# Kernel tuning notes

Measured on AMD Instinct MI355X. Metric: run time of the kernel, lower is better.

Reference implementation:

```python
import jax, jax.numpy as jnp
import numpy as np

H = 16           # num_heads
D = 1024         # num_units
QD = KD = VD = 64
LN_EPS = 1e-5


def _xavier(key, shape):
    fan_in, fan_out = shape[-2], shape[-1]
    std = np.sqrt(2.0 / (fan_in + fan_out))
    return jax.random.normal(key, shape, dtype=jnp.float32) * std


def setup_inputs() -> dict:
    key = jax.random.key(0)
    ks = jax.random.split(key, 10)
    B, Sq, Sk = 8, 1024, 1024
    return {
        "query": jax.random.normal(ks[0], (B, Sq, D), dtype=jnp.float32),
        "keys": jax.random.normal(ks[1], (B, Sk, D), dtype=jnp.float32),
        "values": jax.random.normal(ks[2], (B, Sk, D), dtype=jnp.float32),
        "Wq": _xavier(ks[3], (H, D, QD)),
        "Wk": _xavier(ks[4], (H, D, KD)),
        "Wv": _xavier(ks[5], (H, D, VD)),
        "Wp": _xavier(ks[6], (H * VD, D)),   # proj, stored input-major: y = x @ Wp + bp
        "bp": jnp.zeros((D,), dtype=jnp.float32),
        "gamma": jnp.ones((D,), dtype=jnp.float32),
        "beta": jnp.zeros((D,), dtype=jnp.float32),
    }


def reference(query, keys, values, Wq, Wk, Wv, Wp, bp, gamma, beta):
    B, Sq, _ = query.shape
    Sk = keys.shape[1]
    # RepeatLinear per head: [B,S,D] x [H,D,e] -> [H,B,S,e]
    Q = jnp.einsum("bsd,hde->hbse", query, Wq)
    K = jnp.einsum("bsd,hde->hbse", keys, Wk)
    V = jnp.einsum("bsd,hde->hbse", values, Wv)
    # NOTE: original scales by sqrt(num_units), not sqrt(key_dim)
    temper = jnp.asarray(np.sqrt(D), dtype=Q.dtype)
    scores = jnp.einsum("hbqe,hbke->hbqk", Q, K) / temper  # [H,B,Sq,Sk]
    attn = jax.nn.softmax(scores, axis=-1)
    # dropout is identity in eval mode
    out = jnp.einsum("hbqk,hbke->hbqe", attn, V)           # [H,B,Sq,VD]
    # torch.cat(torch.split(out, B, 0), -1): head-major feature concat
    out = out.transpose(1, 2, 0, 3).reshape(B, Sq, H * VD)
    out = out @ Wp + bp                                     # proj
    # residual + LayerNorm
    y = out + query
    mu = jnp.mean(y, axis=-1, keepdims=True)
    var = jnp.var(y, axis=-1, keepdims=True)
    y = (y - mu) / jnp.sqrt(var + LN_EPS) * gamma + beta
    return y, attn.reshape(H * B, Sq, Sk)
```

## Files before the change

### kernel.cpp

```cpp
#include <hip/hip_runtime.h>
#include <hip/hip_bf16.h>

#define H_ 16
#define B_ 8
#define S_ 1024
#define D_ 1024
#define E_ 64
#define HB_ 128
#define LN_EPS 1e-5f
#define LOG2E 1.4426950408889634f

typedef unsigned short u16;
typedef __bf16 bf16x8 __attribute__((ext_vector_type(8)));
typedef u16 u16x8 __attribute__((ext_vector_type(8)));
typedef u16 u16x4 __attribute__((ext_vector_type(4)));
typedef float f32x4 __attribute__((ext_vector_type(4)));
typedef unsigned u32x2 __attribute__((ext_vector_type(2)));

#define MFMA16(a, b, c) __builtin_amdgcn_mfma_f32_16x16x32_bf16( \
    __builtin_bit_cast(bf16x8, (a)), __builtin_bit_cast(bf16x8, (b)), (c), 0, 0, 0)

#define GLL16(gp, lp) __builtin_amdgcn_global_load_lds( \
    (const __attribute__((address_space(1))) void*)(gp), \
    (__attribute__((address_space(3))) void*)(lp), 16, 0, 0)

__device__ __forceinline__ unsigned cvt_pk_bf16(float lo, float hi) {
  unsigned r;
  asm("v_cvt_pk_bf16_f32 %0, %1, %2" : "=v"(r) : "v"(lo), "v"(hi));
  return r;
}
__device__ __forceinline__ u16x4 pk4(f32x4 v) {
  union { unsigned u[2]; u16x4 s; } r;
  r.u[0] = cvt_pk_bf16(v[0], v[1]);
  r.u[1] = cvt_pk_bf16(v[2], v[3]);
  return r.s;
}
__device__ __forceinline__ float exp2_hw(float x) {
  float r;
  asm("v_exp_f32 %0, %1" : "=v"(r) : "v"(x));
  return r;
}
__device__ __forceinline__ float bfhi(unsigned u) {
  return __builtin_bit_cast(float, u & 0xFFFF0000u);
}
__device__ __forceinline__ float bflo(unsigned u) {
  return __builtin_bit_cast(float, u << 16);
}

__global__ __launch_bounds__(256) void k_prep(
    const float* __restrict__ Wq, const float* __restrict__ Wk,
    const float* __restrict__ Wv, const float* __restrict__ Wp,
    u16* __restrict__ Wt,
    const float* __restrict__ Xq, const float* __restrict__ Xk,
    const float* __restrict__ Xv, u16* __restrict__ Xdst) {
  const int bid = blockIdx.x;
  if (bid >= 1024) {
    const int b2 = bid - 1024;
    const int t = b2 >> 12;
    const float* X = t == 0 ? Xq : t == 1 ? Xk : Xv;
    u16* Y = Xdst + (size_t)t * (8 << 20);
    int i = ((b2 & 4095) * 256 + threadIdx.x) * 8;
    f32x4 a = *(const f32x4*)(X + i);
    f32x4 b = *(const f32x4*)(X + i + 4);
    union { unsigned u[4]; u16x8 s; } v;
    v.u[0] = cvt_pk_bf16(a[0], a[1]);
    v.u[1] = cvt_pk_bf16(a[2], a[3]);
    v.u[2] = cvt_pk_bf16(b[0], b[1]);
    v.u[3] = cvt_pk_bf16(b[2], b[3]);
    *(u16x8*)(Y + i) = v.s;
    return;
  }
  __shared__ float tile[64][65];
  const int which = bid >> 8, r = bid & 255;
  const float* src;
  int R, C, rt, ct;
  float scale = 1.0f;
  size_t soff, doff;
  if (which < 3) {
    src = which == 0 ? Wq : which == 1 ? Wk : Wv;
    if (which == 0) scale = LOG2E / 32.0f;
    int slice = r & 15, rtile = r >> 4;
    R = 1024; C = 64; rt = rtile * 64; ct = 0;
    soff = (size_t)slice * 65536;
    doff = (size_t)which * (1 << 20) + (size_t)slice * 65536;
  } else {
    src = Wp;
    R = 1024; C = 1024; rt = (r & 15) * 64; ct = (r >> 4) * 64;
    soff = 0; doff = (size_t)3 * (1 << 20);
  }
  const float* I = src + soff;
  u16* O = Wt + doff;
  const int t = threadIdx.x;
  const int c4 = (t & 15) * 4;
  #pragma unroll
  for (int i = 0; i < 4; i++) {
    int rr = i * 16 + (t >> 4);
    f32x4 v = *(const f32x4*)&I[(size_t)(rt + rr) * C + ct + c4];
    tile[rr][c4 + 0] = v[0]; tile[rr][c4 + 1] = v[1];
    tile[rr][c4 + 2] = v[2]; tile[rr][c4 + 3] = v[3];
  }
  __syncthreads();
  #pragma unroll
  for (int i = 0; i < 4; i++) {
    int oc = i * 16 + (t >> 4);
    f32x4 tv;
    #pragma unroll
    for (int rr = 0; rr < 4; rr++) tv[rr] = tile[c4 + rr][oc] * scale;
    *(u16x4*)&O[(size_t)(ct + oc) * R + rt + c4] = pk4(tv);
  }
}

#define STAGE_TILES() do { \
    GLL16(Ag + kt,             AsB0); \
    GLL16(Ag + 64 * 1024 + kt, AsB0 + 2048); \
    GLL16(Bg + kt,             BsB0); \
    GLL16(Bg + 64 * 1024 + kt, BsB0 + 2048); \
  } while (0)

#define READ_FRAGS() do { \
    _Pragma("unroll") \
    for (int mi = 0; mi < 4; mi++) \
      af[mi] = *(const u16x8*)&As[(wr * 64 + mi * 16 + lr) * 32 + lg * 8]; \
    _Pragma("unroll") \
    for (int ni = 0; ni < 4; ni++) \
      bf[ni] = *(const u16x8*)&Bs[(wc * 64 + ni * 16 + lr) * 32 + lg * 8]; \
  } while (0)

template<int MODE>
__global__ __launch_bounds__(256) void k_gemm(
    const u16* __restrict__ X0, const u16* __restrict__ Ball,
    u16* __restrict__ O0, u16* __restrict__ O1, u16* __restrict__ O2,
    float* __restrict__ Pf, const float* __restrict__ bp,
    const float* __restrict__ query) {
  const int bid = blockIdx.x + (blockIdx.y << 6);
  const int bx  = ((bid & 7) << 3) + ((bid >> 3) & 7);
  const int by  = bid >> 6;
  const int l  = threadIdx.x & 63;
  const int w  = threadIdx.x >> 6;
  const int lr = l & 15, lg = l >> 4;
  const int wr = w >> 1, wc = w & 1;
  const int m0 = bx * 128, n0 = by * 128;

  const u16* A = (MODE == 0) ? X0 + (size_t)(by >> 3) * (8 << 20) : X0;

  __shared__ __align__(16) u16 As[128 * 32];
  __shared__ __align__(16) u16 Bs[128 * 32];

  const int srow = w * 16 + (l >> 2);
  const int scol = (l & 3) * 8;
  const u16* Ag = A    + (size_t)(m0 + srow) * 1024 + scol;
  const u16* Bg = Ball + (size_t)(n0 + srow) * 1024 + scol;
  u16* AsB0 = As + w * 512;
  u16* BsB0 = Bs + w * 512;

  f32x4 acc[4][4] = {};
  u16x8 af[4], bf[4];

  if (MODE == 2 || by < 16) {
    for (int kt = 0; kt < 1024; kt += 32) {
      STAGE_TILES();
      __syncthreads();
      READ_FRAGS();
      #pragma unroll
      for (int mi = 0; mi < 4; mi++)
        #pragma unroll
        for (int ni = 0; ni < 4; ni++)
          acc[mi][ni] = MFMA16(bf[ni], af[mi], acc[mi][ni]);
      __syncthreads();
    }
  } else {
    for (int kt = 0; kt < 1024; kt += 32) {
      STAGE_TILES();
      __syncthreads();
      READ_FRAGS();
      #pragma unroll
      for (int mi = 0; mi < 4; mi++)
        #pragma unroll
        for (int ni = 0; ni < 4; ni++)
          acc[mi][ni] = MFMA16(af[mi], bf[ni], acc[mi][ni]);
      __syncthreads();
    }
  }

  if (MODE == 0 && by < 16) {
    u16* Out = (by >= 8) ? O1 : O0;
    const int h = (by & 7) * 2 + wc;
    #pragma unroll
    for (int mi = 0; mi < 4; mi++) {
      int s = m0 + wr * 64 + mi * 16 + lr;
      int bb = s >> 10, ss = s & 1023;
      #pragma unroll
      for (int ni = 0; ni < 4; ni++)
        *(u16x4*)&Out[((size_t)(h * 8 + bb) * 1024 + ss) * 64 + ni * 16 + lg * 4] =
            pk4(acc[mi][ni]);
    }
  } else if (MODE == 0) {
    const int byv = by - 16;
    const int h = byv * 2 + wc;
    #pragma unroll
    for (int mi = 0; mi < 4; mi++) {
      int s = m0 + wr * 64 + mi * 16 + lg * 4;
      int bb = s >> 10, ss = s & 1023;
      #pragma unroll
      for (int ni = 0; ni < 4; ni++)
        *(u16x4*)&O2[((size_t)(h * 8 + bb) * 64 + ni * 16 + lr) * 1024 + ss] =
            pk4(acc[mi][ni]);
    }
  } else {
    #pragma unroll
    for (int mi = 0; mi < 4; mi++) {
      int m = m0 + wr * 64 + mi * 16 + lr;
      #pragma unroll
      for (int ni = 0; ni < 4; ni++) {
        int n = n0 + wc * 64 + ni * 16 + lg * 4;
        f32x4 b4 = *(const f32x4*)(bp + n);
        f32x4 q4 = *(const f32x4*)(query + (size_t)m * 1024 + n);
        f32x4 o = acc[mi][ni] + b4 + q4;
        *(f32x4*)(Pf + (size_t)m * 1024 + n) = o;
      }
    }
  }
}

__global__ __launch_bounds__(256, 4) void k_attn(const u16* __restrict__ Qb,
    const u16* __restrict__ Kb, const u16* __restrict__ Vtb,
    float* __restrict__ attn_out, u16* __restrict__ AO) {
  const int bid = blockIdx.x;
  const int xcd = bid & 7, within = bid >> 3;
  const int qt = within & 63;
  const int hb = xcd * 16 + (within >> 6);
  const int w  = threadIdx.x >> 6;
  const int l  = threadIdx.x & 63;
  const int lr = l & 15, lg = l >> 4;
  const int q0 = qt * 16;

  __shared__ __align__(16) u16 pbuf[16 * 1024];
  __shared__ float wmaxs[4][16];
  __shared__ float wsums[4][16];

  const u16* Qp = Qb + ((size_t)hb * 1024 + q0 + lr) * 64 + lg * 8;
  const u16* Kp = Kb + ((size_t)hb * 1024 + w * 256 + lr) * 64 + lg * 8;
  u16x8 q_lo = *(const u16x8*)Qp;
  u16x8 q_hi = *(const u16x8*)(Qp + 32);

  f32x4 sacc[16] = {};
  __builtin_amdgcn_s_setprio(1);
  #pragma unroll
  for (int j = 0; j < 16; j++) {
    u16x8 k0 = *(const u16x8*)(Kp + (size_t)j * 16 * 64);
    u16x8 k1 = *(const u16x8*)(Kp + (size_t)j * 16 * 64 + 32);
    sacc[j] = MFMA16(k0, q_lo, sacc[j]);
    sacc[j] = MFMA16(k1, q_hi, sacc[j]);
  }
  __builtin_amdgcn_s_setprio(0);

  float mx = sacc[0][0];
  #pragma unroll
  for (int j = 0; j < 16; j++)
    #pragma unroll
    for (int r = 0; r < 4; r++) mx = fmaxf(mx, sacc[j][r]);
  mx = fmaxf(mx, __shfl_xor(mx, 16));
  mx = fmaxf(mx, __shfl_xor(mx, 32));

  float sum = 0.f;
  #pragma unroll
  for (int j = 0; j < 16; j++)
    #pragma unroll
    for (int r = 0; r < 4; r++) {
      float p = exp2_hw(sacc[j][r] - mx);
      sacc[j][r] = p;
      sum += p;
    }
  sum += __shfl_xor(sum, 16);
  sum += __shfl_xor(sum, 32);

  const u16* Vp = Vtb + ((size_t)hb * 64 + w * 16 + lr) * 1024 + lg * 8;
  u16x8 vp0 = *(const u16x8*)(Vp + 0);
  u16x8 vp1 = *(const u16x8*)(Vp + 32);
  u16x8 vp2 = *(const u16x8*)(Vp + 64);
  u16x8 vp3 = *(const u16x8*)(Vp + 96);

  #pragma unroll
  for (int j = 0; j < 16; j++) {
    int k0 = w * 256 + j * 16 + lg * 4;
    int byte = (lr * 2048 + k0 * 2) ^ ((lr & 7) << 4);
    *(u16x4*)((char*)pbuf + byte) = pk4(sacc[j]);
  }
  if (l < 16) { wmaxs[w][lr] = mx; wsums[w][lr] = sum; }

  __syncthreads();

  float m0v = wmaxs[0][lr], m1v = wmaxs[1][lr], m2v = wmaxs[2][lr], m3v = wmaxs[3][lr];
  float gmax = fmaxf(fmaxf(m0v, m1v), fmaxf(m2v, m3v));
  float gsum = wsums[0][lr] * exp2_hw(m0v - gmax) + wsums[1][lr] * exp2_hw(m1v - gmax)
             + wsums[2][lr] * exp2_hw(m2v - gmax) + wsums[3][lr] * exp2_hw(m3v - gmax);
  float r01 = exp2_hw(m0v - m1v);
  float r12 = exp2_hw(m1v - m2v);
  float r23 = exp2_hw(m2v - m3v);
  float c3  = exp2_hw(m3v - gmax) / gsum;

  u16x8 vp4 = *(const u16x8*)(Vp + 128);
  u16x8 vp5 = *(const u16x8*)(Vp + 160);
  u16x8 vp6 = *(const u16x8*)(Vp + 192);
  u16x8 vp7 = *(const u16x8*)(Vp + 224);
  u16x8 vq0 = *(const u16x8*)(Vp + 256);
  u16x8 vq1 = *(const u16x8*)(Vp + 288);
  u16x8 vq2 = *(const u16x8*)(Vp + 320);
  u16x8 vq3 = *(const u16x8*)(Vp + 352);
  u16x8 vq4 = *(const u16x8*)(Vp + 384);
  u16x8 vq5 = *(const u16x8*)(Vp + 416);
  u16x8 vq6 = *(const u16x8*)(Vp + 448);
  u16x8 vq7 = *(const u16x8*)(Vp + 480);

  #pragma unroll
  for (int rr = 0; rr < 4; rr++) {
    const int row = w * 4 + rr;
    float M0 = wmaxs[0][row], M1 = wmaxs[1][row], M2 = wmaxs[2][row], M3 = wmaxs[3][row];
    float GM = fmaxf(fmaxf(M0, M1), fmaxf(M2, M3));
    float E0 = exp2_hw(M0 - GM), E1 = exp2_hw(M1 - GM);
    float E2 = exp2_hw(M2 - GM), E3 = exp2_hw(M3 - GM);
    float IV = 1.0f / (wsums[0][row] * E0 + wsums[1][row] * E1 +
                       wsums[2][row] * E2 + wsums[3][row] * E3);
    float cs0 = E0 * IV, cs1 = E1 * IV, cs2 = E2 * IV, cs3 = E3 * IV;
    float* Ap = attn_out + ((size_t)hb * 1024 + q0 + row) * 1024;
    #pragma unroll
    for (int c = 0; c < 4; c++) {
      float sc = c == 0 ? cs0 : c == 1 ? cs1 : c == 2 ? cs2 : cs3;
      int byte = (row * 2048 + (c * 256 + l * 4) * 2) ^ ((row & 7) << 4);
      u32x2 d = *(u32x2*)((char*)pbuf + byte);
      f32x4 v;
      v[0] = bflo(d[0]) * sc;
      v[1] = bfhi(d[0]) * sc;
      v[2] = bflo(d[1]) * sc;
      v[3] = bfhi(d[1]) * sc;
      __builtin_nontemporal_store(v, (f32x4*)(Ap + c * 256 + l * 4));
    }
  }

  f32x4 o = {};
  __builtin_amdgcn_s_setprio(1);
  #define PBUF_P(i, kk) (*(u16x8*)((char*)pbuf + \
      ((lr * 2048 + ((i) * 256 + (kk) * 32 + lg * 8) * 2) ^ ((lr & 7) << 4))))
  o = MFMA16(vp0, PBUF_P(0, 0), o);
  o = MFMA16(vp1, PBUF_P(0, 1), o);
  o = MFMA16(vp2, PBUF_P(0, 2), o);
  o = MFMA16(vp3, PBUF_P(0, 3), o);
  o = MFMA16(vp4, PBUF_P(0, 4), o);
  o = MFMA16(vp5, PBUF_P(0, 5), o);
  o = MFMA16(vp6, PBUF_P(0, 6), o);
  o = MFMA16(vp7, PBUF_P(0, 7), o);
  vp0 = *(const u16x8*)(Vp + 512);
  vp1 = *(const u16x8*)(Vp + 544);
  vp2 = *(const u16x8*)(Vp + 576);
  vp3 = *(const u16x8*)(Vp + 608);
  vp4 = *(const u16x8*)(Vp + 640);
  vp5 = *(const u16x8*)(Vp + 672);
  vp6 = *(const u16x8*)(Vp + 704);
  vp7 = *(const u16x8*)(Vp + 736);
  o *= r01;
  o = MFMA16(vq0, PBUF_P(1, 0), o);
  o = MFMA16(vq1, PBUF_P(1, 1), o);
  o = MFMA16(vq2, PBUF_P(1, 2), o);
  o = MFMA16(vq3, PBUF_P(1, 3), o);
  o = MFMA16(vq4, PBUF_P(1, 4), o);
  o = MFMA16(vq5, PBUF_P(1, 5), o);
  o = MFMA16(vq6, PBUF_P(1, 6), o);
  o = MFMA16(vq7, PBUF_P(1, 7), o);
  vq0 = *(const u16x8*)(Vp + 768);
  vq1 = *(const u16x8*)(Vp + 800);
  vq2 = *(const u16x8*)(Vp + 832);
  vq3 = *(const u16x8*)(Vp + 864);
  vq4 = *(const u16x8*)(Vp + 896);
  vq5 = *(const u16x8*)(Vp + 928);
  vq6 = *(const u16x8*)(Vp + 960);
  vq7 = *(const u16x8*)(Vp + 992);
  o *= r12;
  o = MFMA16(vp0, PBUF_P(2, 0), o);
  o = MFMA16(vp1, PBUF_P(2, 1), o);
  o = MFMA16(vp2, PBUF_P(2, 2), o);
  o = MFMA16(vp3, PBUF_P(2, 3), o);
  o = MFMA16(vp4, PBUF_P(2, 4), o);
  o = MFMA16(vp5, PBUF_P(2, 5), o);
  o = MFMA16(vp6, PBUF_P(2, 6), o);
  o = MFMA16(vp7, PBUF_P(2, 7), o);
  o *= r23;
  o = MFMA16(vq0, PBUF_P(3, 0), o);
  o = MFMA16(vq1, PBUF_P(3, 1), o);
  o = MFMA16(vq2, PBUF_P(3, 2), o);
  o = MFMA16(vq3, PBUF_P(3, 3), o);
  o = MFMA16(vq4, PBUF_P(3, 4), o);
  o = MFMA16(vq5, PBUF_P(3, 5), o);
  o = MFMA16(vq6, PBUF_P(3, 6), o);
  o = MFMA16(vq7, PBUF_P(3, 7), o);
  __builtin_amdgcn_s_setprio(0);
  #undef PBUF_P

  const int bb = hb & 7, hh = hb >> 3;
  f32x4 oc = o * c3;
  *(u16x4*)&AO[((size_t)bb * 1024 + q0 + lr) * 1024 + hh * 64 + w * 16 + lg * 4] = pk4(oc);
}

__global__ __launch_bounds__(256) void k_ln(const float* __restrict__ P,
    const float* __restrict__ gamma, const float* __restrict__ beta,
    float* __restrict__ y) {
  const int row = blockIdx.x * 4 + (threadIdx.x >> 6);
  const int l = threadIdx.x & 63;
  const float* p = P + (size_t)row * 1024 + l * 4;
  f32x4 v[4];
  float s = 0.f, s2 = 0.f;
  #pragma unroll
  for (int i = 0; i < 4; i++) {
    v[i] = *(const f32x4*)(p + i * 256);
    #pragma unroll
    for (int r = 0; r < 4; r++) { s += v[i][r]; s2 += v[i][r] * v[i][r]; }
  }
  #pragma unroll
  for (int off = 1; off < 64; off <<= 1) {
    s += __shfl_xor(s, off);
    s2 += __shfl_xor(s2, off);
  }
  float mu = s * (1.0f / 1024.0f);
  float var = s2 * (1.0f / 1024.0f) - mu * mu;
  float rstd = rsqrtf(var + LN_EPS);
  float* yp = y + (size_t)row * 1024 + l * 4;
  #pragma unroll
  for (int i = 0; i < 4; i++) {
    f32x4 g = *(const f32x4*)(gamma + l * 4 + i * 256);
    f32x4 b = *(const f32x4*)(beta + l * 4 + i * 256);
    f32x4 o;
    #pragma unroll
    for (int r = 0; r < 4; r++) o[r] = (v[i][r] - mu) * rstd * g[r] + b[r];
    __builtin_nontemporal_store(o, (f32x4*)(yp + i * 256));
  }
}

extern "C" void kernel_launch(void* const* d_in, const int* in_sizes, int n_in,
                              void* d_out, int out_size, void* d_ws, size_t ws_size,
                              hipStream_t stream) {
  const float* query  = (const float*)d_in[0];
  const float* keys   = (const float*)d_in[1];
  const float* values = (const float*)d_in[2];
  const float* Wq     = (const float*)d_in[3];
  const float* Wk     = (const float*)d_in[4];
  const float* Wv     = (const float*)d_in[5];
  const float* Wp     = (const float*)d_in[6];
  const float* bp     = (const float*)d_in[7];
  const float* gamma  = (const float*)d_in[8];
  const float* beta   = (const float*)d_in[9];

  float* y        = (float*)d_out;
  float* attn_out = (float*)d_out + (size_t)B_ * S_ * D_;

  u16* ws  = (u16*)d_ws;
  u16* Wqt = ws;
  u16* Wpt = Wqt + (3 << 20);
  u16* Xqb = Wqt + (4 << 20);
  u16* Qb  = Xqb + (24 << 20);
  u16* Kb  = Qb + (8 << 20);
  u16* Vtb = Kb + (8 << 20);
  u16* AO  = Vtb + (8 << 20);
  float* P = (float*)Xqb;

  k_prep<<<13312, 256, 0, stream>>>(Wq, Wk, Wv, Wp, Wqt, query, keys, values, Xqb);

  k_gemm<0><<<dim3(64, 24), 256, 0, stream>>>(Xqb, Wqt, Qb, Kb, Vtb, nullptr, nullptr, nullptr);

  k_attn<<<8192, 256, 0, stream>>>(Qb, Kb, Vtb, attn_out, AO);

  k_gemm<2><<<dim3(64, 8), 256, 0, stream>>>(AO, Wpt, nullptr, nullptr, nullptr, P, bp, query);
  k_ln<<<2048, 256, 0, stream>>>(P, gamma, beta, y);
}
```

Baseline: 388.0 us.

## Split attention kernel into separate PV and score-store kernels

Splits the fused attention kernel into two launches. One computes the softmax and P·V and writes AO. The other recomputes QK^T and the softmax and writes the normalised fp32 attention matrix. The aim is probably to take the large attention-matrix stores out of the PV kernel's critical path and lower register or LDS pressure there. The cost is recomputing the scores and reading Q and K twice.

```diff
diff --git a/kernel.cpp b/kernel.cpp
--- a/kernel.cpp
+++ b/kernel.cpp
@@ -222,9 +222,96 @@
   }
 }
 
-__global__ __launch_bounds__(256, 4) void k_attn(const u16* __restrict__ Qb,
+__global__ __launch_bounds__(256, 4) void k_score(const u16* __restrict__ Qb,
+    const u16* __restrict__ Kb, float* __restrict__ attn_out) {
+  const int bid = blockIdx.x;
+  const int xcd = bid & 7, within = bid >> 3;
+  const int qt = within & 63;
+  const int hb = xcd * 16 + (within >> 6);
+  const int w  = threadIdx.x >> 6;
+  const int l  = threadIdx.x & 63;
+  const int lr = l & 15, lg = l >> 4;
+  const int q0 = qt * 16;
+
+  __shared__ __align__(16) u16 pbuf[16 * 1024];
+  __shared__ float wmaxs[4][16];
+  __shared__ float wsums[4][16];
+
+  const u16* Qp = Qb + ((size_t)hb * 1024 + q0 + lr) * 64 + lg * 8;
+  const u16* Kp = Kb + ((size_t)hb * 1024 + w * 256 + lr) * 64 + lg * 8;
+  u16x8 q_lo = *(const u16x8*)Qp;
+  u16x8 q_hi = *(const u16x8*)(Qp + 32);
+
+  f32x4 sacc[16] = {};
+  __builtin_amdgcn_s_setprio(1);
+  #pragma unroll
+  for (int j = 0; j < 16; j++) {
+    u16x8 k0 = *(const u16x8*)(Kp + (size_t)j * 16 * 64);
+    u16x8 k1 = *(const u16x8*)(Kp + (size_t)j * 16 * 64 + 32);
+    sacc[j] = MFMA16(k0, q_lo, sacc[j]);
+    sacc[j] = MFMA16(k1, q_hi, sacc[j]);
+  }
+  __builtin_amdgcn_s_setprio(0);
+
+  float mx = sacc[0][0];
+  #pragma unroll
+  for (int j = 0; j < 16; j++)
+    #pragma unroll
+    for (int r = 0; r < 4; r++) mx = fmaxf(mx, sacc[j][r]);
+  mx = fmaxf(mx, __shfl_xor(mx, 16));
+  mx = fmaxf(mx, __shfl_xor(mx, 32));
+
+  float sum = 0.f;
+  #pragma unroll
+  for (int j = 0; j < 16; j++)
+    #pragma unroll
+    for (int r = 0; r < 4; r++) {
+      float p = exp2_hw(sacc[j][r] - mx);
+      sacc[j][r] = p;
+      sum += p;
+    }
+  sum += __shfl_xor(sum, 16);
+  sum += __shfl_xor(sum, 32);
+
+  #pragma unroll
+  for (int j = 0; j < 16; j++) {
+    int k0 = w * 256 + j * 16 + lg * 4;
+    int byte = (lr * 2048 + k0 * 2) ^ ((lr & 7) << 4);
+    *(u16x4*)((char*)pbuf + byte) = pk4(sacc[j]);
+  }
+  if (l < 16) { wmaxs[w][lr] = mx; wsums[w][lr] = sum; }
+
+  __syncthreads();
+
+  #pragma unroll
+  for (int rr = 0; rr < 4; rr++) {
+    const int row = w * 4 + rr;
+    float M0 = wmaxs[0][row], M1 = wmaxs[1][row], M2 = wmaxs[2][row], M3 = wmaxs[3][row];
+    float GM = fmaxf(fmaxf(M0, M1), fmaxf(M2, M3));
+    float E0 = exp2_hw(M0 - GM), E1 = exp2_hw(M1 - GM);
+    float E2 = exp2_hw(M2 - GM), E3 = exp2_hw(M3 - GM);
+    float IV = 1.0f / (wsums[0][row] * E0 + wsums[1][row] * E1 +
+                       wsums[2][row] * E2 + wsums[3][row] * E3);
+    float cs0 = E0 * IV, cs1 = E1 * IV, cs2 = E2 * IV, cs3 = E3 * IV;
+    float* Ap = attn_out + ((size_t)hb * 1024 + q0 + row) * 1024;
+    #pragma unroll
+    for (int c = 0; c < 4; c++) {
+      float sc = c == 0 ? cs0 : c == 1 ? cs1 : c == 2 ? cs2 : cs3;
+      int byte = (row * 2048 + (c * 256 + l * 4) * 2) ^ ((row & 7) << 4);
+      u32x2 d = *(u32x2*)((char*)pbuf + byte);
+      f32x4 v;
+      v[0] = bflo(d[0]) * sc;
+      v[1] = bfhi(d[0]) * sc;
+      v[2] = bflo(d[1]) * sc;
+      v[3] = bfhi(d[1]) * sc;
+      __builtin_nontemporal_store(v, (f32x4*)(Ap + c * 256 + l * 4));
+    }
+  }
+}
+
+__global__ __launch_bounds__(256, 4) void k_pv(const u16* __restrict__ Qb,
     const u16* __restrict__ Kb, const u16* __restrict__ Vtb,
-    float* __restrict__ attn_out, u16* __restrict__ AO) {
+    u16* __restrict__ AO) {
   const int bid = blockIdx.x;
   const int xcd = bid & 7, within = bid >> 3;
   const int qt = within & 63;
@@ -311,31 +398,6 @@
   u16x8 vq5 = *(const u16x8*)(Vp + 416);
   u16x8 vq6 = *(const u16x8*)(Vp + 448);
   u16x8 vq7 = *(const u16x8*)(Vp + 480);
-
-  #pragma unroll
-  for (int rr = 0; rr < 4; rr++) {
-    const int row = w * 4 + rr;
-    float M0 = wmaxs[0][row], M1 = wmaxs[1][row], M2 = wmaxs[2][row], M3 = wmaxs[3][row];
-    float GM = fmaxf(fmaxf(M0, M1), fmaxf(M2, M3));
-    float E0 = exp2_hw(M0 - GM), E1 = exp2_hw(M1 - GM);
-    float E2 = exp2_hw(M2 - GM), E3 = exp2_hw(M3 - GM);
-    float IV = 1.0f / (wsums[0][row] * E0 + wsums[1][row] * E1 +
-                       wsums[2][row] * E2 + wsums[3][row] * E3);
-    float cs0 = E0 * IV, cs1 = E1 * IV, cs2 = E2 * IV, cs3 = E3 * IV;
-    float* Ap = attn_out + ((size_t)hb * 1024 + q0 + row) * 1024;
-    #pragma unroll
-    for (int c = 0; c < 4; c++) {
-      float sc = c == 0 ? cs0 : c == 1 ? cs1 : c == 2 ? cs2 : cs3;
-      int byte = (row * 2048 + (c * 256 + l * 4) * 2) ^ ((row & 7) << 4);
-      u32x2 d = *(u32x2*)((char*)pbuf + byte);
-      f32x4 v;
-      v[0] = bflo(d[0]) * sc;
-      v[1] = bfhi(d[0]) * sc;
-      v[2] = bflo(d[1]) * sc;
-      v[3] = bfhi(d[1]) * sc;
-      __builtin_nontemporal_store(v, (f32x4*)(Ap + c * 256 + l * 4));
-    }
-  }
 
   f32x4 o = {};
   __builtin_amdgcn_s_setprio(1);
@@ -465,7 +527,8 @@
 
   k_gemm<0><<<dim3(64, 24), 256, 0, stream>>>(Xqb, Wqt, Qb, Kb, Vtb, nullptr, nullptr, nullptr);
 
-  k_attn<<<8192, 256, 0, stream>>>(Qb, Kb, Vtb, attn_out, AO);
+  k_pv<<<8192, 256, 0, stream>>>(Qb, Kb, Vtb, AO);
+  k_score<<<8192, 256, 0, stream>>>(Qb, Kb, attn_out);
 
   k_gemm<2><<<dim3(64, 8), 256, 0, stream>>>(AO, Wpt, nullptr, nullptr, nullptr, P, bp, query);
   k_ln<<<2048, 256, 0, stream>>>(P, gamma, beta, y);
```

New measurement: 516.8 us. 33.2% more time.
